# Optimization experiments

Measured on AMD Instinct MI355X. Metric: run time of the kernel, lower is better.

## Reference

```python
import math
import numpy as np
import jax, jax.numpy as jnp

LMAX1, LMAX2 = 10, 5
F1, F2 = 20, 40
B_IN, B_L1, B_L2 = 96, 10, 6
ASPECT = 2
BATCH = 32
ACT_CST = math.sqrt(2.0)  # normalize2mom(relu): E[relu(z)^2]=1/2 for z~N(0,1)


def _fact(n):
    return float(math.factorial(n))


def wigner_d_small(l, beta):
    # Wigner small-d matrices, complex-m ordering m=-l..l -> [n, 2l+1, 2l+1]
    beta = np.asarray(beta, dtype=np.float64)
    n = beta.shape[0]
    d = np.zeros((n, 2 * l + 1, 2 * l + 1))
    c, s = np.cos(beta / 2), np.sin(beta / 2)
    for imp, mp in enumerate(range(-l, l + 1)):
        for im, m in enumerate(range(-l, l + 1)):
            pref = math.sqrt(_fact(l + mp) * _fact(l - mp) * _fact(l + m) * _fact(l - m))
            val = np.zeros(n)
            for k in range(max(0, m - mp), min(l + m, l - mp) + 1):
                den = _fact(l + m - k) * _fact(k) * _fact(mp - m + k) * _fact(l - mp - k)
                val += (-1.0) ** (mp - m + k) / den * c ** (2 * l + m - mp - 2 * k) * s ** (mp - m + 2 * k)
            d[:, imp, im] = pref * val
    return d


def U_c2r(l):
    # unitary change of basis complex SH -> real SH, Yr = U @ Yc
    U = np.zeros((2 * l + 1, 2 * l + 1), dtype=np.complex128)
    U[l, l] = 1.0
    sq = 1.0 / math.sqrt(2.0)
    for m in range(1, l + 1):
        cs = (-1.0) ** m
        U[l + m, l + m] = cs * sq
        U[l + m, l - m] = sq
        U[l - m, l + m] = -1j * cs * sq
        U[l - m, l - m] = 1j * sq
    return U


def rot_z_real(l, ang):
    # real-basis rotation about the azimuthal axis -> [n, 2l+1, 2l+1]
    U = U_c2r(l)
    m = np.arange(-l, l + 1)
    ph = np.exp(-1j * np.outer(np.asarray(ang, np.float64), m))
    return np.real(np.einsum('ik,nk,jk->nij', U, ph, U.conj(), optimize=True))


def d_real(l, beta):
    U = U_c2r(l)
    dc = wigner_d_small(l, beta).astype(np.complex128)
    return np.real(np.einsum('ij,njk,lk->nil', U, dc, U.conj(), optimize=True))


def wigner_D_pts(l, a, b, g):
    return np.einsum('nij,njk,nkm->nim', rot_z_real(l, a), d_real(l, b), rot_z_real(l, g), optimize=True)


def flat_wigner_pts(lmax, a, b, g):
    n = len(a)
    return np.concatenate([math.sqrt(2 * l + 1) * wigner_D_pts(l, a, b, g).reshape(n, -1) for l in range(lmax + 1)], -1)


def flat_wigner_grid(lmax, al, be, ga):
    # product grid (alpha x beta x gamma), flattened alpha-major -> [na*nb*ng, sum (2l+1)^2]
    blocks = []
    for l in range(lmax + 1):
        D = np.einsum('aij,bjk,gkm->abgim', rot_z_real(l, al), d_real(l, be), rot_z_real(l, ga), optimize=True)
        blocks.append(math.sqrt(2 * l + 1) * D.reshape(-1, (2 * l + 1) ** 2))
    return np.concatenate(blocks, -1)


def sh_pts(lmax, a, b):
    # component-normalized real SH at points: Y_l = sqrt(2l+1) * D^l(a,b,0)[:, m=0]
    cols = []
    for l in range(lmax + 1):
        M = np.einsum('nij,nj->ni', rot_z_real(l, a), d_real(l, b)[:, :, l], optimize=True)
        cols.append(math.sqrt(2 * l + 1) * M)
    return np.concatenate(cols, -1)


def sh_grid(lmax, al, be):
    # SH on product grid, flattened beta-major to match x.transpose(-1,-2) layout
    cols = []
    for l in range(lmax + 1):
        M = np.einsum('aij,bj->bai', rot_z_real(l, al), d_real(l, be)[:, :, l], optimize=True)
        cols.append(math.sqrt(2 * l + 1) * M.reshape(-1, 2 * l + 1))
    return np.concatenate(cols, -1)


def _so3_grid(res):
    nb, na = 2 * res, 2 * res * ASPECT
    al = 2 * math.pi * np.arange(na) / na
    be = math.pi * (np.arange(nb) + 0.5) / nb
    return al, be, al.copy()


def setup_inputs():
    key = jax.random.key(0)
    k1, k2, k3 = jax.random.split(key, 3)
    # kernel grids (near identity), as in s2/so3_near_identity_grid
    b_s2 = np.arange(1, 4) * (math.pi / 8) / 3
    a_s2 = np.linspace(0, 2 * math.pi, 9)[:-1]
    ga, gb = np.meshgrid(a_s2, b_s2, indexing='ij')
    Yk1 = sh_pts(LMAX1, ga.ravel(), gb.ravel())  # [24, 121]
    a_so3 = np.linspace(0, 2 * math.pi, 8)[:-1]
    g_so3 = np.linspace(-2 * math.pi, 2 * math.pi, 8)
    ga, gb, gg = np.meshgrid(a_so3, b_s2, g_so3, indexing='ij')
    Dk2 = flat_wigner_pts(LMAX2, ga.ravel(), gb.ravel(), gg.ravel())  # [168, 286]
    # FromS2Grid analysis matrix (pinv of band-limited synthesis matrix)
    be = (np.arange(B_IN) + 0.5) / B_IN * math.pi
    al = np.arange(B_IN) / B_IN * 2 * math.pi
    from_s2 = np.linalg.pinv(sh_grid(LMAX1, al, be))  # [121, 9216]
    # SO(3) activation transform matrices
    a1, b1, g1 = _so3_grid(B_L1)
    D1_to = flat_wigner_grid(LMAX1, a1, b1, g1)                     # [32000, 1771]
    F1_from = np.linalg.pinv(flat_wigner_grid(LMAX2, a1, b1, g1))   # [286, 32000]
    a2, b2, g2 = _so3_grid(B_L2)
    D2_to = flat_wigner_grid(LMAX2, a2, b2, g2)                     # [6912, 286]
    F2_from = np.linalg.pinv(flat_wigner_grid(0, a2, b2, g2))       # [1, 6912]
    f32 = lambda v: jnp.asarray(v, dtype=jnp.float32)
    return {
        'x': jax.random.normal(k1, (BATCH, 1, B_IN, B_IN), dtype=jnp.float32),
        'w1': jax.random.normal(k2, (1, F1, Yk1.shape[0]), dtype=jnp.float32),
        'w2': jax.random.normal(k3, (F1, F2, Dk2.shape[0]), dtype=jnp.float32),
        'Yk1': f32(Yk1), 'Dk2': f32(Dk2), 'from_s2': f32(from_s2),
        'D1_to': f32(D1_to), 'F1_from': f32(F1_from),
        'D2_to': f32(D2_to), 'F2_from': f32(F2_from),
    }


def reference(x, w1, w2, Yk1, Dk2, from_s2, D1_to, F1_from, D2_to, F2_from):
    B = x.shape[0]
    # [B,1,alpha,beta] -> [B,1,beta,alpha] -> S2 Fourier coefficients
    c = jnp.einsum('bfg,cg->bfc', jnp.swapaxes(x, -1, -2).reshape(B, 1, -1), from_s2)  # [B,1,121]
    # S2 -> SO(3) convolution (e3nn Linear with SH-built weights)
    psi1 = jnp.einsum('ni,xyn->xyi', Yk1, w1) / math.sqrt(Yk1.shape[0])  # [1,F1,121]
    outs = []
    for l in range(LMAX1 + 1):
        k = 2 * l + 1
        ol = jnp.einsum('bim,ijn->bjnm', c[:, :, l * l:l * l + k], psi1[:, :, l * l:l * l + k])  # fan_in = 1
        outs.append(ol.reshape(B, F1, k * k))
    h = jnp.concatenate(outs, -1)  # [B,F1,1771]
    # SO(3) activation: Fourier -> grid, relu, grid -> Fourier (lmax 10 -> 5)
    g = ACT_CST * jax.nn.relu(jnp.einsum('bfc,gc->bfg', h, D1_to))
    h = jnp.einsum('bfg,cg->bfc', g, F1_from)  # [B,F1,286]
    # SO(3) -> SO(3) convolution (Wigner-D-built weights)
    psi2 = jnp.einsum('nc,xyn->xyc', Dk2, w2) / math.sqrt(Dk2.shape[0])  # [F1,F2,286]
    outs, off = [], 0
    for l in range(LMAX2 + 1):
        k = 2 * l + 1
        xl = h[:, :, off:off + k * k].reshape(B, F1, k, k)       # [B,i,u,m]
        pl = psi2[:, :, off:off + k * k].reshape(F1, F2, k, k)   # [i,j,u,v]
        ol = jnp.einsum('bium,ijuv->bjvm', xl, pl) / math.sqrt(F1 * k)  # fan_in = F1*(2l+1)
        outs.append(ol.reshape(B, F2, k * k))
        off += k * k
    h = jnp.concatenate(outs, -1)  # [B,F2,286]
    # final SO(3) activation lmax 5 -> 0
    g = ACT_CST * jax.nn.relu(jnp.einsum('bfc,gc->bfg', h, D2_to))
    return jnp.einsum('bfg,cg->bfc', g, F2_from)  # [B,F2,1]
```

## Files before the change

### kernel.cpp

```cpp
#include <hip/hip_runtime.h>
#include <hip/hip_bf16.h>
#include <math.h>


#define B_      32
#define F1_     20
#define F2_     40
#define NC1     1771
#define K1P     1792
#define NG1     32000
#define NC2     286
#define K2P     288
#define NG2     6912
#define SQRT2_  1.41421356237309515f
#define RS24    0.20412414523193154f
#define RS168   0.07715167498104595f

typedef unsigned int   uint32;
typedef unsigned short u16;
typedef __attribute__((ext_vector_type(8))) short short8;
typedef __attribute__((ext_vector_type(4))) float f32x4;

#define AS1(p) ((const __attribute__((address_space(1))) void*)(p))
#define AS3(p) ((__attribute__((address_space(3))) void*)(p))

__device__ __forceinline__ u16 f2bf(float f) {
  uint32 u = __float_as_uint(f);
  return (u16)((u + 0x7FFFu + ((u >> 16) & 1u)) >> 16);
}
__device__ __forceinline__ uint32 pack_bf16(float lo, float hi) {
  uint32 a = __float_as_uint(lo), b = __float_as_uint(hi);
  a = (a + 0x7FFFu + ((a >> 16) & 1u)) >> 16;
  b = (b + 0x7FFFu + ((b >> 16) & 1u)) & 0xFFFF0000u;
  return a | b;
}

__device__ __forceinline__ float wave_reduce(float v) {
#pragma unroll
  for (int o = 32; o > 0; o >>= 1) v += __shfl_down(v, o, 64);
  return v;
}


__global__ void k_c(const float* __restrict__ x, const float* __restrict__ fs,
                    float* __restrict__ c) {
  const int ch = blockIdx.x, b = blockIdx.y, tid = threadIdx.x;
  const float* xb = x + b * 9216;
  const float* fr = fs + ch * 9216;
  float s = 0.f;
  for (int g = tid; g < 9216; g += 256) {
    s += xb[(g % 96) * 96 + (g / 96)] * fr[g];
  }
  s = wave_reduce(s);
  __shared__ float red[4];
  if ((tid & 63) == 0) red[tid >> 6] = s;
  __syncthreads();
  if (tid == 0) c[b * 121 + ch] = red[0] + red[1] + red[2] + red[3];
}

__global__ void k_psi1(const float* __restrict__ Yk1, const float* __restrict__ w1,
                       float* __restrict__ psi1) {
  const int j = blockIdx.x, i = threadIdx.x;
  __shared__ float wsm[24];
  if (i < 24) wsm[i] = w1[j * 24 + i];
  __syncthreads();
  if (i < 121) {
    float s = 0.f;
#pragma unroll
    for (int n = 0; n < 24; ++n) s += Yk1[n * 121 + i] * wsm[n];
    psi1[j * 121 + i] = s * RS24;
  }
}

__global__ void k_h(const float* __restrict__ c, const float* __restrict__ psi1,
                    u16* __restrict__ hb) {
  const int j = blockIdx.x, b = blockIdx.y, tid = threadIdx.x;
  __shared__ float cs[121], ps[121];
  if (tid < 121) { cs[tid] = c[b * 121 + tid]; ps[tid] = psi1[j * 121 + tid]; }
  __syncthreads();
  for (int idx = tid; idx < K1P; idx += 256) {
    u16 v = 0;
    if (idx < NC1) {
      int off = 0, l = 0, k = 1;
      while (idx >= off + k * k) { off += k * k; ++l; k += 2; }
      const int r = idx - off, n = r / k, m = r % k;
      v = f2bf(cs[l * l + m] * ps[l * l + n]);
    }
    hb[(size_t)(b * F1_ + j) * K1P + idx] = v;
  }
}


__global__ void k_cvt1(const float* __restrict__ in, uint32* __restrict__ out) {
  const int total = 32000 * 896;
  for (int id = blockIdx.x * 256 + threadIdx.x; id < total; id += gridDim.x * 256) {
    const int r = id / 896, c2 = id % 896, cc = c2 * 2;
    const float* p = in + (size_t)r * NC1 + cc;
    const float lo = (cc < NC1) ? p[0] : 0.f;
    const float hi = (cc + 1 < NC1) ? p[1] : 0.f;
    out[id] = pack_bf16(lo, hi);
  }
}

__global__ void k_cvt2(const float* __restrict__ in, uint32* __restrict__ out) {
  const int total = 286 * 16000;
  for (int id = blockIdx.x * 256 + threadIdx.x; id < total; id += gridDim.x * 256) {
    out[id] = pack_bf16(in[2 * id], in[2 * id + 1]);
  }
}

__global__ void k_cvt3(const float* __restrict__ in, uint32* __restrict__ out) {
  const int total = 6912 * 144;
  for (int id = blockIdx.x * 256 + threadIdx.x; id < total; id += gridDim.x * 256) {
    const int r = id / 144, c2 = id % 144, cc = c2 * 2;
    const float* p = in + (size_t)r * NC2 + cc;
    const float lo = (cc < NC2) ? p[0] : 0.f;
    const float hi = (cc + 1 < NC2) ? p[1] : 0.f;
    out[id] = pack_bf16(lo, hi);
  }
}


__launch_bounds__(256)
__global__ void k_gemm1_v3(const u16* __restrict__ A, const u16* __restrict__ B,
                           u16* __restrict__ C) {
  __shared__ __align__(16) u16 As[128 * 32];
  __shared__ __align__(16) u16 Bs[128 * 32];
  const int bid = blockIdx.x;
  const int g = bid / 40, loc = bid % 40;
  int nt, mt;
  if (g < 31) { nt = g * 8 + (loc & 7); mt = loc >> 3; }
  else        { nt = 248 + (loc & 1);  mt = loc >> 1; }
  const int m0 = mt * 128, n0 = nt * 128;
  const int tid = threadIdx.x;
  const int lane = tid & 63, w = tid >> 6;
  const int wm = w >> 1, wn = w & 1;
  const int q = lane >> 4, r16 = lane & 15;

  f32x4 acc[4][4] = {};
  const u16* ag = A + (size_t)(m0 + (tid >> 2)) * K1P + (tid & 3) * 8;
  const u16* bg = B + (size_t)(n0 + (tid >> 2)) * K1P + (tid & 3) * 8;

  for (int k0 = 0; k0 < K1P; k0 += 32) {
#pragma unroll
    for (int i = 0; i < 2; ++i) {
      __builtin_amdgcn_global_load_lds(AS1(ag + k0 + (size_t)i * 64 * K1P),
                                       AS3((char*)As + i * 4096 + w * 1024), 16, 0, 0);
      __builtin_amdgcn_global_load_lds(AS1(bg + k0 + (size_t)i * 64 * K1P),
                                       AS3((char*)Bs + i * 4096 + w * 1024), 16, 0, 0);
    }
    __syncthreads();
    short8 af[4], bf[4];
#pragma unroll
    for (int mb = 0; mb < 4; ++mb)
      af[mb] = *(const short8*)&As[(wm * 64 + mb * 16 + r16) * 32 + q * 8];
#pragma unroll
    for (int nb = 0; nb < 4; ++nb)
      bf[nb] = *(const short8*)&Bs[(wn * 64 + nb * 16 + r16) * 32 + q * 8];
#pragma unroll
    for (int mb = 0; mb < 4; ++mb)
#pragma unroll
      for (int nb = 0; nb < 4; ++nb)
        acc[mb][nb] = __builtin_amdgcn_mfma_f32_16x16x32_bf16(af[mb], bf[nb], acc[mb][nb], 0, 0, 0);
    __syncthreads();
  }
#pragma unroll
  for (int mb = 0; mb < 4; ++mb) {
#pragma unroll
    for (int nb = 0; nb < 4; ++nb) {
      const int col = n0 + wn * 64 + nb * 16 + r16;
#pragma unroll
      for (int r = 0; r < 4; ++r) {
        const int row = m0 + wm * 64 + mb * 16 + q * 4 + r;
        float v = acc[mb][nb][r];
        v = (v > 0.f) ? v * SQRT2_ : 0.f;
        C[(size_t)row * NG1 + col] = f2bf(v);
      }
    }
  }
}

__launch_bounds__(256)
__global__ void k_gemm2_v3(const u16* __restrict__ A, const u16* __restrict__ B,
                           float* __restrict__ C) {
  __shared__ __align__(16) u16 As[128 * 32];
  __shared__ __align__(16) u16 Bs[128 * 32];
  const int m0 = blockIdx.x * 128, n0 = blockIdx.y * 128;
  const int ks = blockIdx.z * 1600;
  const int tid = threadIdx.x;
  const int lane = tid & 63, w = tid >> 6;
  const int wm = w >> 1, wn = w & 1;
  const int q = lane >> 4, r16 = lane & 15;

  f32x4 acc[4][4] = {};
  const u16* ag = A + (size_t)(m0 + (tid >> 2)) * NG1 + ks + (tid & 3) * 8;
  int rb0 = n0 + (tid >> 2);        if (rb0 > 285) rb0 = 285;
  int rb1 = n0 + (tid >> 2) + 64;   if (rb1 > 285) rb1 = 285;
  const u16* bg0 = B + (size_t)rb0 * NG1 + ks + (tid & 3) * 8;
  const u16* bg1 = B + (size_t)rb1 * NG1 + ks + (tid & 3) * 8;

  for (int kt = 0; kt < 1600; kt += 32) {
#pragma unroll
    for (int i = 0; i < 2; ++i) {
      __builtin_amdgcn_global_load_lds(AS1(ag + kt + (size_t)i * 64 * NG1),
                                       AS3((char*)As + i * 4096 + w * 1024), 16, 0, 0);
    }
    __builtin_amdgcn_global_load_lds(AS1(bg0 + kt), AS3((char*)Bs + w * 1024), 16, 0, 0);
    __builtin_amdgcn_global_load_lds(AS1(bg1 + kt), AS3((char*)Bs + 4096 + w * 1024), 16, 0, 0);
    __syncthreads();
    short8 af[4], bf[4];
#pragma unroll
    for (int mb = 0; mb < 4; ++mb)
      af[mb] = *(const short8*)&As[(wm * 64 + mb * 16 + r16) * 32 + q * 8];
#pragma unroll
    for (int nb = 0; nb < 4; ++nb)
      bf[nb] = *(const short8*)&Bs[(wn * 64 + nb * 16 + r16) * 32 + q * 8];
#pragma unroll
    for (int mb = 0; mb < 4; ++mb)
#pragma unroll
      for (int nb = 0; nb < 4; ++nb)
        acc[mb][nb] = __builtin_amdgcn_mfma_f32_16x16x32_bf16(af[mb], bf[nb], acc[mb][nb], 0, 0, 0);
    __syncthreads();
  }
#pragma unroll
  for (int mb = 0; mb < 4; ++mb) {
#pragma unroll
    for (int nb = 0; nb < 4; ++nb) {
      const int col = n0 + wn * 64 + nb * 16 + r16;
      if (col < NC2) {
#pragma unroll
        for (int r = 0; r < 4; ++r) {
          const int row = m0 + wm * 64 + mb * 16 + q * 4 + r;
          atomicAdd(&C[(size_t)row * NC2 + col], acc[mb][nb][r]);
        }
      }
    }
  }
}

__launch_bounds__(256)
__global__ void k_gemm3_v3(const u16* __restrict__ A, const u16* __restrict__ B,
                           const float* __restrict__ wv, float* __restrict__ out) {
  __shared__ __align__(16) u16 As[128 * 32];
  __shared__ __align__(16) u16 Bs[128 * 32];
  __shared__ float red[128][33];
  const int m0 = blockIdx.x * 128, n0 = blockIdx.y * 128;
  const int tid = threadIdx.x;
  const int lane = tid & 63, w = tid >> 6;
  const int wm = w >> 1, wn = w & 1;
  const int q = lane >> 4, r16 = lane & 15;

  f32x4 acc[4][4] = {};
  const u16* ag = A + (size_t)(m0 + (tid >> 2)) * K2P + (tid & 3) * 8;
  const u16* bg = B + (size_t)(n0 + (tid >> 2)) * K2P + (tid & 3) * 8;

  for (int k0 = 0; k0 < K2P; k0 += 32) {
#pragma unroll
    for (int i = 0; i < 2; ++i) {
      __builtin_amdgcn_global_load_lds(AS1(ag + k0 + (size_t)i * 64 * K2P),
                                       AS3((char*)As + i * 4096 + w * 1024), 16, 0, 0);
      __builtin_amdgcn_global_load_lds(AS1(bg + k0 + (size_t)i * 64 * K2P),
                                       AS3((char*)Bs + i * 4096 + w * 1024), 16, 0, 0);
    }
    __syncthreads();
    short8 af[4], bf[4];
#pragma unroll
    for (int mb = 0; mb < 4; ++mb)
      af[mb] = *(const short8*)&As[(wm * 64 + mb * 16 + r16) * 32 + q * 8];
#pragma unroll
    for (int nb = 0; nb < 4; ++nb)
      bf[nb] = *(const short8*)&Bs[(wn * 64 + nb * 16 + r16) * 32 + q * 8];
#pragma unroll
    for (int mb = 0; mb < 4; ++mb)
#pragma unroll
      for (int nb = 0; nb < 4; ++nb)
        acc[mb][nb] = __builtin_amdgcn_mfma_f32_16x16x32_bf16(af[mb], bf[nb], acc[mb][nb], 0, 0, 0);
    __syncthreads();
  }
  float wvv[4];
#pragma unroll
  for (int nb = 0; nb < 4; ++nb) wvv[nb] = wv[n0 + wn * 64 + nb * 16 + r16];
#pragma unroll
  for (int mb = 0; mb < 4; ++mb) {
#pragma unroll
    for (int r = 0; r < 4; ++r) {
      const int rowl = wm * 64 + mb * 16 + q * 4 + r;
      float t = 0.f;
#pragma unroll
      for (int nb = 0; nb < 4; ++nb) {
        float v = acc[mb][nb][r];
        v = (v > 0.f) ? v : 0.f;
        t += v * wvv[nb];
      }
      red[rowl][wn * 16 + r16] = t;
    }
  }
  __syncthreads();
  if (tid < 128) {
    float s = 0.f;
#pragma unroll
    for (int cc = 0; cc < 32; ++cc) s += red[tid][cc];
    atomicAdd(&out[m0 + tid], s * SQRT2_);
  }
}


__launch_bounds__(256)
__global__ void k_gemm1_mfma(const u16* __restrict__ A, const float* __restrict__ Bf,
                             u16* __restrict__ C) {
  __shared__ __align__(16) u16 As[128 * 32];
  __shared__ __align__(16) u16 Bs[128 * 32];
  const int tid = threadIdx.x;
  const int lane = tid & 63, w = tid >> 6;
  const int wm = w >> 1, wn = w & 1;
  const int q = lane >> 4, r16 = lane & 15;
  const int m0 = blockIdx.x * 128, n0 = blockIdx.y * 128;

  f32x4 acc[4][4] = {};
  const u16* ag = A + (size_t)(m0 + (tid >> 2)) * K1P + (tid & 3) * 8;

  for (int k0 = 0; k0 < K1P; k0 += 32) {
#pragma unroll
    for (int i = 0; i < 2; ++i) {
      __builtin_amdgcn_global_load_lds(AS1(ag + k0 + (size_t)i * 64 * K1P),
                                       AS3((char*)As + i * 4096 + w * 1024), 16, 0, 0);
    }
#pragma unroll
    for (int i = 0; i < 8; ++i) {
      const int p = i * 256 + tid;
      const int row = p >> 4, c2 = (p & 15) * 2;
      const int kk = k0 + c2;
      const float* bp = Bf + (size_t)(n0 + row) * NC1 + kk;
      const float lo = (kk < NC1) ? bp[0] : 0.f;
      const float hi = (kk + 1 < NC1) ? bp[1] : 0.f;
      ((uint32*)Bs)[row * 16 + (p & 15)] = pack_bf16(lo, hi);
    }
    __syncthreads();
    short8 af[4], bf[4];
#pragma unroll
    for (int mb = 0; mb < 4; ++mb)
      af[mb] = *(const short8*)&As[(wm * 64 + mb * 16 + r16) * 32 + q * 8];
#pragma unroll
    for (int nb = 0; nb < 4; ++nb)
      bf[nb] = *(const short8*)&Bs[(wn * 64 + nb * 16 + r16) * 32 + q * 8];
#pragma unroll
    for (int mb = 0; mb < 4; ++mb)
#pragma unroll
      for (int nb = 0; nb < 4; ++nb)
        acc[mb][nb] = __builtin_amdgcn_mfma_f32_16x16x32_bf16(af[mb], bf[nb], acc[mb][nb], 0, 0, 0);
    __syncthreads();
  }
#pragma unroll
  for (int mb = 0; mb < 4; ++mb) {
#pragma unroll
    for (int nb = 0; nb < 4; ++nb) {
      const int col = n0 + wn * 64 + nb * 16 + r16;
#pragma unroll
      for (int r = 0; r < 4; ++r) {
        const int row = m0 + wm * 64 + mb * 16 + q * 4 + r;
        float v = acc[mb][nb][r];
        v = (v > 0.f) ? v * SQRT2_ : 0.f;
        C[(size_t)row * NG1 + col] = f2bf(v);
      }
    }
  }
}

__launch_bounds__(256)
__global__ void k_gemm2_mfma(const u16* __restrict__ A, const float* __restrict__ Bf,
                             float* __restrict__ C) {
  __shared__ __align__(16) u16 As[128 * 32];
  __shared__ __align__(16) u16 Bs[128 * 32];
  const int tid = threadIdx.x;
  const int lane = tid & 63, w = tid >> 6;
  const int wm = w >> 1, wn = w & 1;
  const int q = lane >> 4, r16 = lane & 15;
  const int m0 = blockIdx.x * 128, n0 = blockIdx.y * 128;
  const int ks = blockIdx.z * 1600;

  f32x4 acc[4][4] = {};
  const u16* ag = A + (size_t)(m0 + (tid >> 2)) * NG1 + ks + (tid & 3) * 8;

  for (int kt = 0; kt < 1600; kt += 32) {
#pragma unroll
    for (int i = 0; i < 2; ++i) {
      __builtin_amdgcn_global_load_lds(AS1(ag + kt + (size_t)i * 64 * NG1),
                                       AS3((char*)As + i * 4096 + w * 1024), 16, 0, 0);
    }
#pragma unroll
    for (int i = 0; i < 4; ++i) {
      const int idx = i * 256 + tid;
      const int row = idx >> 3, c4 = (idx & 7) * 4;
      const int n = n0 + row;
      float4 v = make_float4(0.f, 0.f, 0.f, 0.f);
      if (n < NC2) v = *(const float4*)(Bf + (size_t)n * NG1 + ks + kt + c4);
      ((uint32*)Bs)[row * 16 + (idx & 7) * 2]     = pack_bf16(v.x, v.y);
      ((uint32*)Bs)[row * 16 + (idx & 7) * 2 + 1] = pack_bf16(v.z, v.w);
    }
    __syncthreads();
    short8 af[4], bf[4];
#pragma unroll
    for (int mb = 0; mb < 4; ++mb)
      af[mb] = *(const short8*)&As[(wm * 64 + mb * 16 + r16) * 32 + q * 8];
#pragma unroll
    for (int nb = 0; nb < 4; ++nb)
      bf[nb] = *(const short8*)&Bs[(wn * 64 + nb * 16 + r16) * 32 + q * 8];
#pragma unroll
    for (int mb = 0; mb < 4; ++mb)
#pragma unroll
      for (int nb = 0; nb < 4; ++nb)
        acc[mb][nb] = __builtin_amdgcn_mfma_f32_16x16x32_bf16(af[mb], bf[nb], acc[mb][nb], 0, 0, 0);
    __syncthreads();
  }
#pragma unroll
  for (int mb = 0; mb < 4; ++mb) {
#pragma unroll
    for (int nb = 0; nb < 4; ++nb) {
      const int col = n0 + wn * 64 + nb * 16 + r16;
      if (col < NC2) {
#pragma unroll
        for (int r = 0; r < 4; ++r) {
          const int row = m0 + wm * 64 + mb * 16 + q * 4 + r;
          atomicAdd(&C[(size_t)row * NC2 + col], acc[mb][nb][r]);
        }
      }
    }
  }
}


__global__ void k_psi2(const float* __restrict__ Dk2, const float* __restrict__ w2,
                       float* __restrict__ psi2) {
  const int blk = blockIdx.x, tid = threadIdx.x;
  __shared__ float w2s[168];
  if (tid < 168) w2s[tid] = w2[blk * 168 + tid];
  __syncthreads();
  for (int cc = tid; cc < NC2; cc += 256) {
    float s = 0.f;
    for (int n = 0; n < 168; ++n) s += Dk2[n * NC2 + cc] * w2s[n];
    psi2[blk * NC2 + cc] = s * RS168;
  }
}

__global__ void k_step7(const float* __restrict__ h2, const float* __restrict__ psi2,
                        u16* __restrict__ h3b) {
  const int j = blockIdx.x, b = blockIdx.y, tid = threadIdx.x;
  __shared__ float sh[20 * 286];
  __shared__ float sp[20 * 286];
  for (int e = tid; e < 20 * 286; e += 256) {
    const int i = e / 286, cc = e % 286;
    sh[e] = h2[(b * F1_ + i) * NC2 + cc];
    sp[e] = psi2[(i * F2_ + j) * NC2 + cc];
  }
  __syncthreads();
  for (int cidx = tid; cidx < K2P; cidx += 256) {
    u16 ov = 0;
    if (cidx < NC2) {
      int off = 0, l = 0, k = 1;
      while (cidx >= off + k * k) { off += k * k; ++l; k += 2; }
      const int r = cidx - off, v = r / k, m = r % k;
      float acc = 0.f;
      for (int i = 0; i < 20; ++i) {
        const float* hbp = &sh[i * 286 + off];
        const float* pb = &sp[i * 286 + off];
        for (int u = 0; u < k; ++u) acc += hbp[u * k + m] * pb[u * k + v];
      }
      ov = f2bf(acc * rsqrtf(20.f * (float)k));
    }
    h3b[(size_t)(b * F2_ + j) * K2P + cidx] = ov;
  }
}


extern "C" void kernel_launch(void* const* d_in, const int* in_sizes, int n_in,
                              void* d_out, int out_size, void* d_ws, size_t ws_size,
                              hipStream_t stream) {
  const float* x       = (const float*)d_in[0];
  const float* w1      = (const float*)d_in[1];
  const float* w2      = (const float*)d_in[2];
  const float* Yk1     = (const float*)d_in[3];
  const float* Dk2     = (const float*)d_in[4];
  const float* from_s2 = (const float*)d_in[5];
  const float* D1_to   = (const float*)d_in[6];
  const float* F1_from = (const float*)d_in[7];
  const float* D2_to   = (const float*)d_in[8];
  const float* F2_from = (const float*)d_in[9];
  float* out = (float*)d_out;

  float* ws = (float*)d_ws;
  float* c    = ws + 0;
  float* psi1 = ws + 3872;
  float* h2   = ws + 6292;
  float* psi2 = ws + 189332;
  u16*   h3b  = (u16*)(ws + 418132);
  u16*   hb   = (u16*)(ws + 602452);
  u16*   g    = (u16*)(ws + 1175892);
  u16*   D2bf = (u16*)(ws + 11415892);
  u16*   F1bf = (u16*)(ws + 12411220);
  u16*   D1bf = (u16*)(ws + 16987220);
  const size_t BIG_NEED = (size_t)45659220 * 4;
  const bool big = ws_size >= BIG_NEED;

  k_c   <<<dim3(121, 32), 256, 0, stream>>>(x, from_s2, c);
  k_psi1<<<dim3(20),      128, 0, stream>>>(Yk1, w1, psi1);
  k_h   <<<dim3(20, 32),  256, 0, stream>>>(c, psi1, hb);
  k_cvt3<<<dim3(1024),    256, 0, stream>>>(D2_to, (uint32*)D2bf);

  if (big) {
    k_cvt1<<<dim3(8192), 256, 0, stream>>>(D1_to, (uint32*)D1bf);
    k_cvt2<<<dim3(4096), 256, 0, stream>>>(F1_from, (uint32*)F1bf);
    k_gemm1_v3<<<dim3(1250), 256, 0, stream>>>(hb, D1bf, g);
    hipMemsetAsync(h2, 0, (size_t)640 * 286 * sizeof(float), stream);
    k_gemm2_v3<<<dim3(5, 3, 20), 256, 0, stream>>>(g, F1bf, h2);
  } else {
    k_gemm1_mfma<<<dim3(5, 250), 256, 0, stream>>>(hb, D1_to, g);
    hipMemsetAsync(h2, 0, (size_t)640 * 286 * sizeof(float), stream);
    k_gemm2_mfma<<<dim3(5, 3, 20), 256, 0, stream>>>(g, F1_from, h2);
  }

  k_psi2 <<<dim3(800),    256, 0, stream>>>(Dk2, w2, psi2);
  k_step7<<<dim3(40, 32), 256, 0, stream>>>(h2, psi2, h3b);

  hipMemsetAsync(out, 0, (size_t)1280 * sizeof(float), stream);
  k_gemm3_v3<<<dim3(10, 54), 256, 0, stream>>>(h3b, D2bf, F2_from, out);
}
```

Baseline: 776.1 us.

## Triple-buffer LDS in the two big GEMMs and pre-transpose x for coalesced projection

The two large bf16 MFMA GEMMs move from single-buffered LDS with two barriers per K step to a three-stage ring. Loads are issued two tiles ahead, and each stage does a vmcnt wait plus one barrier, so global-to-LDS traffic overlaps the MFMA work. Separately, x is transposed once through a shared-memory tile so the S2 projection reads contiguous float4 data instead of strided gathers. The cost is three times the LDS per block, which may lower occupancy, plus a hand-encoded waitcnt value whose correctness depends on the instruction encoding.

```diff
diff --git a/kernel.cpp b/kernel.cpp
--- a/kernel.cpp
+++ b/kernel.cpp
@@ -24,6 +24,8 @@
 #define AS1(p) ((const __attribute__((address_space(1))) void*)(p))
 #define AS3(p) ((__attribute__((address_space(3))) void*)(p))
 
+#define WAITCNT_VM4 0x0F74
+
 __device__ __forceinline__ u16 f2bf(float f) {
   uint32 u = __float_as_uint(f);
   return (u16)((u + 0x7FFFu + ((u >> 16) & 1u)) >> 16);
@@ -41,6 +43,43 @@
   return v;
 }
 
+
+__global__ void k_xt(const float* __restrict__ x, float* __restrict__ xt) {
+  __shared__ float t[32][33];
+  const int b = blockIdx.z, i0 = blockIdx.x * 32, j0 = blockIdx.y * 32;
+  const int tx = threadIdx.x & 31, ty0 = threadIdx.x >> 5;
+  const float* xb = x + b * 9216;
+  float* xtb = xt + b * 9216;
+#pragma unroll
+  for (int r = 0; r < 4; ++r) {
+    const int ty = ty0 + r * 8;
+    t[ty][tx] = xb[(i0 + ty) * 96 + j0 + tx];
+  }
+  __syncthreads();
+#pragma unroll
+  for (int r = 0; r < 4; ++r) {
+    const int ty = ty0 + r * 8;
+    xtb[(j0 + ty) * 96 + i0 + tx] = t[tx][ty];
+  }
+}
+
+__global__ void k_c2(const float* __restrict__ xt, const float* __restrict__ fs,
+                     float* __restrict__ c) {
+  const int ch = blockIdx.x, b = blockIdx.y, tid = threadIdx.x;
+  const float4* xb = (const float4*)(xt + b * 9216);
+  const float4* fr = (const float4*)(fs + ch * 9216);
+  float s = 0.f;
+#pragma unroll 3
+  for (int g = tid; g < 2304; g += 256) {
+    const float4 a = xb[g], d = fr[g];
+    s += a.x * d.x + a.y * d.y + a.z * d.z + a.w * d.w;
+  }
+  s = wave_reduce(s);
+  __shared__ float red[4];
+  if ((tid & 63) == 0) red[tid >> 6] = s;
+  __syncthreads();
+  if (tid == 0) c[b * 121 + ch] = red[0] + red[1] + red[2] + red[3];
+}
 
 __global__ void k_c(const float* __restrict__ x, const float* __restrict__ fs,
                     float* __restrict__ c) {
@@ -122,48 +161,72 @@
 
 
 __launch_bounds__(256)
-__global__ void k_gemm1_v3(const u16* __restrict__ A, const u16* __restrict__ B,
+__global__ void k_gemm1_v4(const u16* __restrict__ A, const u16* __restrict__ B,
                            u16* __restrict__ C) {
-  __shared__ __align__(16) u16 As[128 * 32];
-  __shared__ __align__(16) u16 Bs[128 * 32];
+  __shared__ __align__(16) u16 As0[128 * 32], As1[128 * 32], As2[128 * 32];
+  __shared__ __align__(16) u16 Bs0[128 * 32], Bs1[128 * 32], Bs2[128 * 32];
   const int bid = blockIdx.x;
-  const int g = bid / 40, loc = bid % 40;
+  const int gg = bid / 40, loc = bid % 40;
   int nt, mt;
-  if (g < 31) { nt = g * 8 + (loc & 7); mt = loc >> 3; }
-  else        { nt = 248 + (loc & 1);  mt = loc >> 1; }
+  if (gg < 31) { nt = gg * 8 + (loc & 7); mt = loc >> 3; }
+  else         { nt = 248 + (loc & 1);   mt = loc >> 1; }
   const int m0 = mt * 128, n0 = nt * 128;
   const int tid = threadIdx.x;
   const int lane = tid & 63, w = tid >> 6;
   const int wm = w >> 1, wn = w & 1;
   const int q = lane >> 4, r16 = lane & 15;
 
-  f32x4 acc[4][4] = {};
   const u16* ag = A + (size_t)(m0 + (tid >> 2)) * K1P + (tid & 3) * 8;
   const u16* bg = B + (size_t)(n0 + (tid >> 2)) * K1P + (tid & 3) * 8;
 
-  for (int k0 = 0; k0 < K1P; k0 += 32) {
-#pragma unroll
-    for (int i = 0; i < 2; ++i) {
-      __builtin_amdgcn_global_load_lds(AS1(ag + k0 + (size_t)i * 64 * K1P),
-                                       AS3((char*)As + i * 4096 + w * 1024), 16, 0, 0);
-      __builtin_amdgcn_global_load_lds(AS1(bg + k0 + (size_t)i * 64 * K1P),
-                                       AS3((char*)Bs + i * 4096 + w * 1024), 16, 0, 0);
-    }
-    __syncthreads();
-    short8 af[4], bf[4];
-#pragma unroll
-    for (int mb = 0; mb < 4; ++mb)
-      af[mb] = *(const short8*)&As[(wm * 64 + mb * 16 + r16) * 32 + q * 8];
-#pragma unroll
-    for (int nb = 0; nb < 4; ++nb)
-      bf[nb] = *(const short8*)&Bs[(wn * 64 + nb * 16 + r16) * 32 + q * 8];
-#pragma unroll
-    for (int mb = 0; mb < 4; ++mb)
-#pragma unroll
-      for (int nb = 0; nb < 4; ++nb)
-        acc[mb][nb] = __builtin_amdgcn_mfma_f32_16x16x32_bf16(af[mb], bf[nb], acc[mb][nb], 0, 0, 0);
-    __syncthreads();
-  }
+#define G1_ISSUE(kk, Asb, Bsb)                                                   \
+  {                                                                              \
+    _Pragma("unroll")                                                            \
+    for (int i = 0; i < 2; ++i) {                                                \
+      __builtin_amdgcn_global_load_lds(AS1(ag + (kk) * 32 + (size_t)i * 64 * K1P), \
+          AS3((char*)(Asb) + i * 4096 + w * 1024), 16, 0, 0);                    \
+      __builtin_amdgcn_global_load_lds(AS1(bg + (kk) * 32 + (size_t)i * 64 * K1P), \
+          AS3((char*)(Bsb) + i * 4096 + w * 1024), 16, 0, 0);                    \
+    }                                                                            \
+  }
+
+#define G1_COMPUTE(Asb, Bsb)                                                     \
+  {                                                                              \
+    short8 af[4], bq[4];                                                         \
+    _Pragma("unroll")                                                            \
+    for (int mb = 0; mb < 4; ++mb)                                               \
+      af[mb] = *(const short8*)&(Asb)[(wm * 64 + mb * 16 + r16) * 32 + q * 8];   \
+    _Pragma("unroll")                                                            \
+    for (int nb = 0; nb < 4; ++nb)                                               \
+      bq[nb] = *(const short8*)&(Bsb)[(wn * 64 + nb * 16 + r16) * 32 + q * 8];   \
+    _Pragma("unroll")                                                            \
+    for (int mb = 0; mb < 4; ++mb)                                               \
+      _Pragma("unroll")                                                          \
+      for (int nb = 0; nb < 4; ++nb)                                             \
+        acc[mb][nb] = __builtin_amdgcn_mfma_f32_16x16x32_bf16(af[mb], bq[nb],    \
+                                                              acc[mb][nb], 0, 0, 0); \
+  }
+
+#define G1_STAGE(kk, AsR, BsR, AsI, BsI)        \
+  {                                             \
+    __builtin_amdgcn_s_waitcnt(WAITCNT_VM4);    \
+    __builtin_amdgcn_s_barrier();               \
+    asm volatile("" ::: "memory");              \
+    if ((kk) + 2 < 56) G1_ISSUE((kk) + 2, AsI, BsI) \
+    G1_COMPUTE(AsR, BsR)                        \
+  }
+
+  f32x4 acc[4][4] = {};
+  G1_ISSUE(0, As0, Bs0)
+  G1_ISSUE(1, As1, Bs1)
+  for (int k = 0; k < 54; k += 3) {
+    G1_STAGE(k,     As0, Bs0, As2, Bs2)
+    G1_STAGE(k + 1, As1, Bs1, As0, Bs0)
+    G1_STAGE(k + 2, As2, Bs2, As1, Bs1)
+  }
+  G1_STAGE(54, As0, Bs0, As2, Bs2)
+  G1_STAGE(55, As1, Bs1, As0, Bs0)
+
 #pragma unroll
   for (int mb = 0; mb < 4; ++mb) {
 #pragma unroll
@@ -178,13 +241,16 @@
       }
     }
   }
+#undef G1_ISSUE
+#undef G1_COMPUTE
+#undef G1_STAGE
 }
 
 __launch_bounds__(256)
-__global__ void k_gemm2_v3(const u16* __restrict__ A, const u16* __restrict__ B,
+__global__ void k_gemm2_v4(const u16* __restrict__ A, const u16* __restrict__ B,
                            float* __restrict__ C) {
-  __shared__ __align__(16) u16 As[128 * 32];
-  __shared__ __align__(16) u16 Bs[128 * 32];
+  __shared__ __align__(16) u16 As0[128 * 32], As1[128 * 32], As2[128 * 32];
+  __shared__ __align__(16) u16 Bs0[128 * 32], Bs1[128 * 32], Bs2[128 * 32];
   const int m0 = blockIdx.x * 128, n0 = blockIdx.y * 128;
   const int ks = blockIdx.z * 1600;
   const int tid = threadIdx.x;
@@ -192,36 +258,61 @@
   const int wm = w >> 1, wn = w & 1;
   const int q = lane >> 4, r16 = lane & 15;
 
-  f32x4 acc[4][4] = {};
   const u16* ag = A + (size_t)(m0 + (tid >> 2)) * NG1 + ks + (tid & 3) * 8;
   int rb0 = n0 + (tid >> 2);        if (rb0 > 285) rb0 = 285;
   int rb1 = n0 + (tid >> 2) + 64;   if (rb1 > 285) rb1 = 285;
   const u16* bg0 = B + (size_t)rb0 * NG1 + ks + (tid & 3) * 8;
   const u16* bg1 = B + (size_t)rb1 * NG1 + ks + (tid & 3) * 8;
 
-  for (int kt = 0; kt < 1600; kt += 32) {
-#pragma unroll
-    for (int i = 0; i < 2; ++i) {
-      __builtin_amdgcn_global_load_lds(AS1(ag + kt + (size_t)i * 64 * NG1),
-                                       AS3((char*)As + i * 4096 + w * 1024), 16, 0, 0);
-    }
-    __builtin_amdgcn_global_load_lds(AS1(bg0 + kt), AS3((char*)Bs + w * 1024), 16, 0, 0);
-    __builtin_amdgcn_global_load_lds(AS1(bg1 + kt), AS3((char*)Bs + 4096 + w * 1024), 16, 0, 0);
-    __syncthreads();
-    short8 af[4], bf[4];
-#pragma unroll
-    for (int mb = 0; mb < 4; ++mb)
-      af[mb] = *(const short8*)&As[(wm * 64 + mb * 16 + r16) * 32 + q * 8];
-#pragma unroll
-    for (int nb = 0; nb < 4; ++nb)
-      bf[nb] = *(const short8*)&Bs[(wn * 64 + nb * 16 + r16) * 32 + q * 8];
-#pragma unroll
-    for (int mb = 0; mb < 4; ++mb)
-#pragma unroll
-      for (int nb = 0; nb < 4; ++nb)
-        acc[mb][nb] = __builtin_amdgcn_mfma_f32_16x16x32_bf16(af[mb], bf[nb], acc[mb][nb], 0, 0, 0);
-    __syncthreads();
-  }
+#define G2_ISSUE(kk, Asb, Bsb)                                                   \
+  {                                                                              \
+    _Pragma("unroll")                                                            \
+    for (int i = 0; i < 2; ++i)                                                  \
+      __builtin_amdgcn_global_load_lds(AS1(ag + (kk) * 32 + (size_t)i * 64 * NG1), \
+          AS3((char*)(Asb) + i * 4096 + w * 1024), 16, 0, 0);                    \
+    __builtin_amdgcn_global_load_lds(AS1(bg0 + (kk) * 32),                       \
+        AS3((char*)(Bsb) + w * 1024), 16, 0, 0);                                 \
+    __builtin_amdgcn_global_load_lds(AS1(bg1 + (kk) * 32),                       \
+        AS3((char*)(Bsb) + 4096 + w * 1024), 16, 0, 0);                          \
+  }
+
+#define G2_COMPUTE(Asb, Bsb)                                                     \
+  {                                                                              \
+    short8 af[4], bq[4];                                                         \
+    _Pragma("unroll")                                                            \
+    for (int mb = 0; mb < 4; ++mb)                                               \
+      af[mb] = *(const short8*)&(Asb)[(wm * 64 + mb * 16 + r16) * 32 + q * 8];   \
+    _Pragma("unroll")                                                            \
+    for (int nb = 0; nb < 4; ++nb)                                               \
+      bq[nb] = *(const short8*)&(Bsb)[(wn * 64 + nb * 16 + r16) * 32 + q * 8];   \
+    _Pragma("unroll")                                                            \
+    for (int mb = 0; mb < 4; ++mb)                                               \
+      _Pragma("unroll")                                                          \
+      for (int nb = 0; nb < 4; ++nb)                                             \
+        acc[mb][nb] = __builtin_amdgcn_mfma_f32_16x16x32_bf16(af[mb], bq[nb],    \
+                                                              acc[mb][nb], 0, 0, 0); \
+  }
+
+#define G2_STAGE(kk, AsR, BsR, AsI, BsI)        \
+  {                                             \
+    __builtin_amdgcn_s_waitcnt(WAITCNT_VM4);    \
+    __builtin_amdgcn_s_barrier();               \
+    asm volatile("" ::: "memory");              \
+    if ((kk) + 2 < 50) G2_ISSUE((kk) + 2, AsI, BsI) \
+    G2_COMPUTE(AsR, BsR)                        \
+  }
+
+  f32x4 acc[4][4] = {};
+  G2_ISSUE(0, As0, Bs0)
+  G2_ISSUE(1, As1, Bs1)
+  for (int k = 0; k < 48; k += 3) {
+    G2_STAGE(k,     As0, Bs0, As2, Bs2)
+    G2_STAGE(k + 1, As1, Bs1, As0, Bs0)
+    G2_STAGE(k + 2, As2, Bs2, As1, Bs1)
+  }
+  G2_STAGE(48, As0, Bs0, As2, Bs2)
+  G2_STAGE(49, As1, Bs1, As0, Bs0)
+
 #pragma unroll
   for (int mb = 0; mb < 4; ++mb) {
 #pragma unroll
@@ -236,6 +327,9 @@
       }
     }
   }
+#undef G2_ISSUE
+#undef G2_COMPUTE
+#undef G2_STAGE
 }
 
 __launch_bounds__(256)
@@ -263,18 +357,18 @@
                                        AS3((char*)Bs + i * 4096 + w * 1024), 16, 0, 0);
     }
     __syncthreads();
-    short8 af[4], bf[4];
+    short8 af[4], bq[4];
 #pragma unroll
     for (int mb = 0; mb < 4; ++mb)
       af[mb] = *(const short8*)&As[(wm * 64 + mb * 16 + r16) * 32 + q * 8];
 #pragma unroll
     for (int nb = 0; nb < 4; ++nb)
-      bf[nb] = *(const short8*)&Bs[(wn * 64 + nb * 16 + r16) * 32 + q * 8];
+      bq[nb] = *(const short8*)&Bs[(wn * 64 + nb * 16 + r16) * 32 + q * 8];
 #pragma unroll
     for (int mb = 0; mb < 4; ++mb)
 #pragma unroll
       for (int nb = 0; nb < 4; ++nb)
-        acc[mb][nb] = __builtin_amdgcn_mfma_f32_16x16x32_bf16(af[mb], bf[nb], acc[mb][nb], 0, 0, 0);
+        acc[mb][nb] = __builtin_amdgcn_mfma_f32_16x16x32_bf16(af[mb], bq[nb], acc[mb][nb], 0, 0, 0);
     __syncthreads();
   }
   float wvv[4];
@@ -336,18 +430,18 @@
       ((uint32*)Bs)[row * 16 + (p & 15)] = pack_bf16(lo, hi);
     }
     __syncthreads();
-    short8 af[4], bf[4];
+    short8 af[4], bq[4];
 #pragma unroll
     for (int mb = 0; mb < 4; ++mb)
       af[mb] = *(const short8*)&As[(wm * 64 + mb * 16 + r16) * 32 + q * 8];
 #pragma unroll
     for (int nb = 0; nb < 4; ++nb)
-      bf[nb] = *(const short8*)&Bs[(wn * 64 + nb * 16 + r16) * 32 + q * 8];
+      bq[nb] = *(const short8*)&Bs[(wn * 64 + nb * 16 + r16) * 32 + q * 8];
 #pragma unroll
     for (int mb = 0; mb < 4; ++mb)
 #pragma unroll
       for (int nb = 0; nb < 4; ++nb)
-        acc[mb][nb] = __builtin_amdgcn_mfma_f32_16x16x32_bf16(af[mb], bf[nb], acc[mb][nb], 0, 0, 0);
+        acc[mb][nb] = __builtin_amdgcn_mfma_f32_16x16x32_bf16(af[mb], bq[nb], acc[mb][nb], 0, 0, 0);
     __syncthreads();
   }
 #pragma unroll
@@ -398,18 +492,18 @@
       ((uint32*)Bs)[row * 16 + (idx & 7) * 2 + 1] = pack_bf16(v.z, v.w);
     }
     __syncthreads();
-    short8 af[4], bf[4];
+    short8 af[4], bq[4];
 #pragma unroll
     for (int mb = 0; mb < 4; ++mb)
       af[mb] = *(const short8*)&As[(wm * 64 + mb * 16 + r16) * 32 + q * 8];
 #pragma unroll
     for (int nb = 0; nb < 4; ++nb)
-      bf[nb] = *(const short8*)&Bs[(wn * 64 + nb * 16 + r16) * 32 + q * 8];
+      bq[nb] = *(const short8*)&Bs[(wn * 64 + nb * 16 + r16) * 32 + q * 8];
 #pragma unroll
     for (int mb = 0; mb < 4; ++mb)
 #pragma unroll
       for (int nb = 0; nb < 4; ++nb)
-        acc[mb][nb] = __builtin_amdgcn_mfma_f32_16x16x32_bf16(af[mb], bf[nb], acc[mb][nb], 0, 0, 0);
+        acc[mb][nb] = __builtin_amdgcn_mfma_f32_16x16x32_bf16(af[mb], bq[nb], acc[mb][nb], 0, 0, 0);
     __syncthreads();
   }
 #pragma unroll
@@ -498,10 +592,18 @@
   u16*   D2bf = (u16*)(ws + 11415892);
   u16*   F1bf = (u16*)(ws + 12411220);
   u16*   D1bf = (u16*)(ws + 16987220);
+  float* x_t  = ws + 45659220;
   const size_t BIG_NEED = (size_t)45659220 * 4;
-  const bool big = ws_size >= BIG_NEED;
-
-  k_c   <<<dim3(121, 32), 256, 0, stream>>>(x, from_s2, c);
+  const size_t XT_NEED  = (size_t)45954132 * 4;
+  const bool big   = ws_size >= BIG_NEED;
+  const bool useXT = ws_size >= XT_NEED;
+
+  if (useXT) {
+    k_xt<<<dim3(3, 3, 32), 256, 0, stream>>>(x, x_t);
+    k_c2<<<dim3(121, 32),  256, 0, stream>>>(x_t, from_s2, c);
+  } else {
+    k_c <<<dim3(121, 32),  256, 0, stream>>>(x, from_s2, c);
+  }
   k_psi1<<<dim3(20),      128, 0, stream>>>(Yk1, w1, psi1);
   k_h   <<<dim3(20, 32),  256, 0, stream>>>(c, psi1, hb);
   k_cvt3<<<dim3(1024),    256, 0, stream>>>(D2_to, (uint32*)D2bf);
@@ -509,9 +611,9 @@
   if (big) {
     k_cvt1<<<dim3(8192), 256, 0, stream>>>(D1_to, (uint32*)D1bf);
     k_cvt2<<<dim3(4096), 256, 0, stream>>>(F1_from, (uint32*)F1bf);
-    k_gemm1_v3<<<dim3(1250), 256, 0, stream>>>(hb, D1bf, g);
+    k_gemm1_v4<<<dim3(1250), 256, 0, stream>>>(hb, D1bf, g);
     hipMemsetAsync(h2, 0, (size_t)640 * 286 * sizeof(float), stream);
-    k_gemm2_v3<<<dim3(5, 3, 20), 256, 0, stream>>>(g, F1bf, h2);
+    k_gemm2_v4<<<dim3(5, 3, 20), 256, 0, stream>>>(g, F1bf, h2);
   } else {
     k_gemm1_mfma<<<dim3(5, 250), 256, 0, stream>>>(hb, D1_to, g);
     hipMemsetAsync(h2, 0, (size_t)640 * 286 * sizeof(float), stream);
```

Result: faster. 674.8 us (-13.1%).
